# Performance work log

Hardware: AMD Instinct MI355X
Metric: run time of the kernel (lower is better)

## Reference

```python
import jax, jax.numpy as jnp
import numpy as np

B, N, D_IN, D_OUT, MAX_POS = 256, 256, 768, 300, 256
NEG_INF = -9e15
LEAKY_SLOPE = 0.2


def setup_inputs() -> dict:
    key = jax.random.key(0)
    ks = jax.random.split(key, 6)
    h = jax.random.normal(ks[0], (B, N, D_IN), dtype=jnp.float32)
    adj = (jax.random.uniform(ks[1], (B, N, N)) > 0.9).astype(jnp.float32)
    adj = jnp.maximum(adj, jnp.eye(N, dtype=jnp.float32)[None])
    positions = jax.random.randint(ks[2], (B, N), 0, MAX_POS)
    W = jax.random.normal(ks[3], (D_IN, D_OUT), dtype=jnp.float32) * (1.0 / np.sqrt(D_IN))
    a_src = jax.random.normal(ks[4], (1, D_OUT), dtype=jnp.float32) * 0.05
    a_dst = jax.random.normal(ks[5], (1, D_OUT), dtype=jnp.float32) * 0.05
    pos_table = jax.random.normal(jax.random.fold_in(key, 7), (MAX_POS, D_OUT), dtype=jnp.float32)
    return {"h": h, "adj": adj, "positions": positions, "W": W,
            "a_src": a_src, "a_dst": a_dst, "pos_table": pos_table}


def reference(h, adj, positions, W, a_src, a_dst, pos_table):
    # Wh = W(h) + position embedding          [B, N, D_OUT]
    Wh = jnp.einsum('bni,io->bno', h, W) + pos_table[positions]
    # additive attention scores
    f_src = jnp.einsum('bno,o->bn', Wh, a_src[0])  # [B, N]
    f_dst = jnp.einsum('bno,o->bn', Wh, a_dst[0])  # [B, N]
    e = f_src[:, :, None] + f_dst[:, None, :]      # [B, N, N]
    e = jnp.where(e >= 0, e, LEAKY_SLOPE * e)      # LeakyReLU(0.2)
    # adjacency masking + softmax over last dim
    masked = jnp.where(adj > 0, e, NEG_INF)
    attention = jax.nn.softmax(masked, axis=-1)
    # (eval mode: edge dropout and dropout are identity)
    h_prime = jnp.einsum('bnm,bmo->bno', attention, Wh)
    return h_prime, attention
```

## Files before the change

### kernel.cpp

```cpp
#include <hip/hip_runtime.h>

#define B_    256
#define N_    256
#define DIN   768
#define DOUT  300
#define DOUTP 320
#define NT    20
#define M_    (B_*N_)
#define HP_ELEMS (M_*DOUT)
#define NEG_INF -9.0e15f

typedef _Float16 f16;
typedef __attribute__((ext_vector_type(8))) _Float16 f16x8;
typedef __attribute__((ext_vector_type(4))) _Float16 f16x4;
typedef __attribute__((ext_vector_type(4))) float    f32x4;

__device__ __forceinline__ void async_copy16(void* lds, const void* g) {
    __builtin_amdgcn_global_load_lds(
        (const __attribute__((address_space(1))) void*)g,
        (__attribute__((address_space(3))) void*)lds, 16, 0, 0);
}

__global__ __launch_bounds__(256) void prep_wt(const float* __restrict__ W,
                                               f16* __restrict__ Wt) {
    int idx = blockIdx.x * 256 + threadIdx.x;
    if (idx >= DOUTP * DIN) return;
    int n = idx / DIN, k = idx - n * DIN;
    float v = (n < DOUT) ? W[k * DOUT + n] : 0.0f;
    Wt[idx] = (f16)v;
}

__global__ __launch_bounds__(256, 3) void gemm1(
    const float* __restrict__ h, const f16* __restrict__ Wt,
    const int* __restrict__ positions,
    const float* __restrict__ a_src, const float* __restrict__ a_dst,
    const float* __restrict__ pos_table,
    f16* __restrict__ WhT, float* __restrict__ f_src, float* __restrict__ f_dst)
{
    __shared__ f16 Al[64 * 40];
    __shared__ f16 Bl[DOUTP * 32];
    __shared__ float pfs[64][2], pfd[64][2];

    const int tid  = threadIdx.x;
    const int wave = tid >> 6, lane = tid & 63;
    const int quad = lane >> 4, c = lane & 15;
    const int rh = wave & 1;
    const int chf = wave >> 1;
    const int rowbase = blockIdx.x * 64;

    const int brow = lane >> 2;
    const int bj   = (lane & 3) ^ (brow & 3);

    const int ar = tid >> 2, aj = tid & 3;

    f32x4 acc[2][10];
#pragma unroll
    for (int rt = 0; rt < 2; ++rt)
#pragma unroll
        for (int i = 0; i < 10; ++i) acc[rt][i] = (f32x4){0.f, 0.f, 0.f, 0.f};

    for (int kt = 0; kt < DIN / 32; ++kt) {
#pragma unroll
        for (int i = 0; i < 5; ++i) {
            int chk = wave + 4 * i;
            int n = chk * 16 + brow;
            async_copy16((char*)Bl + chk * 1024,
                         Wt + (size_t)n * DIN + kt * 32 + bj * 8);
        }
        {
            const float4* src = (const float4*)(h + (size_t)(rowbase + ar) * DIN + kt * 32 + aj * 8);
            float4 v0 = src[0], v1 = src[1];
            *(f16x8*)&Al[ar * 40 + aj * 8] =
                (f16x8){(f16)v0.x, (f16)v0.y, (f16)v0.z, (f16)v0.w,
                        (f16)v1.x, (f16)v1.y, (f16)v1.z, (f16)v1.w};
        }
        __syncthreads();

        f16x8 af0 = *(const f16x8*)&Al[(rh * 32 + c) * 40 + quad * 8];
        f16x8 af1 = *(const f16x8*)&Al[(rh * 32 + 16 + c) * 40 + quad * 8];
#pragma unroll
        for (int i = 0; i < 10; ++i) {
            int n = (chf * 10 + i) * 16 + c;
            f16x8 bf = *(const f16x8*)&Bl[n * 32 + (quad ^ (n & 3)) * 8];
            acc[0][i] = __builtin_amdgcn_mfma_f32_16x16x32_f16(af0, bf, acc[0][i], 0, 0, 0);
            acc[1][i] = __builtin_amdgcn_mfma_f32_16x16x32_f16(af1, bf, acc[1][i], 0, 0, 0);
        }
        __syncthreads();
    }

    const int bidx  = rowbase >> 8;
    const int mloc  = (rowbase & 255);

    int posr[2][4];
#pragma unroll
    for (int rt = 0; rt < 2; ++rt)
#pragma unroll
        for (int r = 0; r < 4; ++r)
            posr[rt][r] = positions[rowbase + rh * 32 + rt * 16 + quad * 4 + r];

    float fs[2][4] = {{0,0,0,0},{0,0,0,0}}, fd[2][4] = {{0,0,0,0},{0,0,0,0}};
#pragma unroll
    for (int i = 0; i < 10; ++i) {
        int col = (chf * 10 + i) * 16 + c;
        if (col < DOUT) {
            float as = a_src[col], ad = a_dst[col];
#pragma unroll
            for (int rt = 0; rt < 2; ++rt)
#pragma unroll
                for (int r = 0; r < 4; ++r) {
                    float v = acc[rt][i][r] + pos_table[posr[rt][r] * DOUT + col];
                    acc[rt][i][r] = v;
                    fs[rt][r] += v * as;
                    fd[rt][r] += v * ad;
                }
        } else {
#pragma unroll
            for (int rt = 0; rt < 2; ++rt)
#pragma unroll
                for (int r = 0; r < 4; ++r) acc[rt][i][r] = 0.0f;
        }
    }
#pragma unroll
    for (int off = 1; off < 16; off <<= 1) {
#pragma unroll
        for (int rt = 0; rt < 2; ++rt)
#pragma unroll
            for (int r = 0; r < 4; ++r) {
                fs[rt][r] += __shfl_xor(fs[rt][r], off, 16);
                fd[rt][r] += __shfl_xor(fd[rt][r], off, 16);
            }
    }
    if (c == 0) {
#pragma unroll
        for (int rt = 0; rt < 2; ++rt)
#pragma unroll
            for (int r = 0; r < 4; ++r) {
                int row = rh * 32 + rt * 16 + quad * 4 + r;
                pfs[row][chf] = fs[rt][r];
                pfd[row][chf] = fd[rt][r];
            }
    }
#pragma unroll
    for (int i = 0; i < 10; ++i) {
        int col = (chf * 10 + i) * 16 + c;
#pragma unroll
        for (int rt = 0; rt < 2; ++rt) {
            int mrow = mloc + rh * 32 + rt * 16 + quad * 4;
            f16x4 u = (f16x4){(f16)acc[rt][i][0], (f16)acc[rt][i][1],
                              (f16)acc[rt][i][2], (f16)acc[rt][i][3]};
            *(f16x4*)(WhT + ((size_t)bidx * DOUTP + col) * N_ + mrow) = u;
        }
    }
    __syncthreads();
    if (tid < 64) {
        f_src[rowbase + tid] = pfs[tid][0] + pfs[tid][1];
        f_dst[rowbase + tid] = pfd[tid][0] + pfd[tid][1];
    }
}

__global__ __launch_bounds__(256) void softmax_att(
    const float* __restrict__ adj, const float* __restrict__ f_src,
    const float* __restrict__ f_dst, float* __restrict__ att)
{
    const int wave = threadIdx.x >> 6, lane = threadIdx.x & 63;
    const int row = blockIdx.x * 4 + wave;
    const int b = row >> 8;

    float fs = f_src[row];
    float4 fd4 = *(const float4*)(f_dst + b * N_ + lane * 4);
    float4 a4  = *(const float4*)(adj + (size_t)row * N_ + lane * 4);

    float e[4];
    {
        float v;
        v = fs + fd4.x; v = v >= 0.f ? v : 0.2f * v; e[0] = a4.x > 0.f ? v : NEG_INF;
        v = fs + fd4.y; v = v >= 0.f ? v : 0.2f * v; e[1] = a4.y > 0.f ? v : NEG_INF;
        v = fs + fd4.z; v = v >= 0.f ? v : 0.2f * v; e[2] = a4.z > 0.f ? v : NEG_INF;
        v = fs + fd4.w; v = v >= 0.f ? v : 0.2f * v; e[3] = a4.w > 0.f ? v : NEG_INF;
    }
    float mx = fmaxf(fmaxf(e[0], e[1]), fmaxf(e[2], e[3]));
#pragma unroll
    for (int off = 1; off < 64; off <<= 1) mx = fmaxf(mx, __shfl_xor(mx, off, 64));

    float p[4], s = 0.f;
#pragma unroll
    for (int i = 0; i < 4; ++i) { p[i] = __expf(e[i] - mx); s += p[i]; }
#pragma unroll
    for (int off = 1; off < 64; off <<= 1) s += __shfl_xor(s, off, 64);

    float inv = 1.0f / s;
    *(float4*)(att + (size_t)row * N_ + lane * 4) =
        make_float4(p[0] * inv, p[1] * inv, p[2] * inv, p[3] * inv);
}

__global__ __launch_bounds__(256, 3) void gemm2(
    const float* __restrict__ att, const f16* __restrict__ WhT,
    float* __restrict__ hp)
{
    __shared__ f16 Al[64 * 40];
    __shared__ f16 Bl[DOUTP * 32];

    const int tid  = threadIdx.x;
    const int wave = tid >> 6, lane = tid & 63;
    const int quad = lane >> 4, c = lane & 15;
    const int rh = wave & 1;
    const int chf = wave >> 1;
    const int rowbase = blockIdx.x * 64;
    const int bidx = rowbase >> 8;

    const int brow = lane >> 2;
    const int bj   = (lane & 3) ^ (brow & 3);
    const int ar = tid >> 2, aj = tid & 3;

    f32x4 acc[2][10];
#pragma unroll
    for (int rt = 0; rt < 2; ++rt)
#pragma unroll
        for (int i = 0; i < 10; ++i) acc[rt][i] = (f32x4){0.f, 0.f, 0.f, 0.f};

    for (int kt = 0; kt < N_ / 32; ++kt) {
#pragma unroll
        for (int i = 0; i < 5; ++i) {
            int chk = wave + 4 * i;
            int n = chk * 16 + brow;
            async_copy16((char*)Bl + chk * 1024,
                         WhT + ((size_t)bidx * DOUTP + n) * N_ + kt * 32 + bj * 8);
        }
        {
            const float4* src = (const float4*)(att + (size_t)(rowbase + ar) * N_ + kt * 32 + aj * 8);
            float4 v0 = src[0], v1 = src[1];
            *(f16x8*)&Al[ar * 40 + aj * 8] =
                (f16x8){(f16)v0.x, (f16)v0.y, (f16)v0.z, (f16)v0.w,
                        (f16)v1.x, (f16)v1.y, (f16)v1.z, (f16)v1.w};
        }
        __syncthreads();

        f16x8 af0 = *(const f16x8*)&Al[(rh * 32 + c) * 40 + quad * 8];
        f16x8 af1 = *(const f16x8*)&Al[(rh * 32 + 16 + c) * 40 + quad * 8];
#pragma unroll
        for (int i = 0; i < 10; ++i) {
            int n = (chf * 10 + i) * 16 + c;
            f16x8 bf = *(const f16x8*)&Bl[n * 32 + (quad ^ (n & 3)) * 8];
            acc[0][i] = __builtin_amdgcn_mfma_f32_16x16x32_f16(af0, bf, acc[0][i], 0, 0, 0);
            acc[1][i] = __builtin_amdgcn_mfma_f32_16x16x32_f16(af1, bf, acc[1][i], 0, 0, 0);
        }
        __syncthreads();
    }

#pragma unroll
    for (int i = 0; i < 10; ++i) {
        int col = (chf * 10 + i) * 16 + c;
        if (col < DOUT) {
#pragma unroll
            for (int rt = 0; rt < 2; ++rt) {
                int row0 = rowbase + rh * 32 + rt * 16 + quad * 4;
#pragma unroll
                for (int r = 0; r < 4; ++r)
                    hp[(size_t)(row0 + r) * DOUT + col] = acc[rt][i][r];
            }
        }
    }
}

extern "C" void kernel_launch(void* const* d_in, const int* in_sizes, int n_in,
                              void* d_out, int out_size, void* d_ws, size_t ws_size,
                              hipStream_t stream)
{
    const float* h         = (const float*)d_in[0];
    const float* adj       = (const float*)d_in[1];
    const int*   positions = (const int*)d_in[2];
    const float* W         = (const float*)d_in[3];
    const float* a_src     = (const float*)d_in[4];
    const float* a_dst     = (const float*)d_in[5];
    const float* pos_table = (const float*)d_in[6];

    float* hp  = (float*)d_out;
    float* att = hp + HP_ELEMS;

    f16*   Wt    = (f16*)d_ws;
    f16*   WhT   = Wt + (size_t)DOUTP * DIN;
    float* f_src = (float*)(WhT + (size_t)B_ * DOUTP * N_);
    float* f_dst = f_src + M_;

    hipLaunchKernelGGL(prep_wt,     dim3((DOUTP * DIN + 255) / 256), dim3(256), 0, stream, W, Wt);
    hipLaunchKernelGGL(gemm1,       dim3(M_ / 64),  dim3(256), 0, stream,
                       h, Wt, positions, a_src, a_dst, pos_table, WhT, f_src, f_dst);
    hipLaunchKernelGGL(softmax_att, dim3(M_ / 4),   dim3(256), 0, stream, adj, f_src, f_dst, att);
    hipLaunchKernelGGL(gemm2,       dim3(M_ / 64),  dim3(256), 0, stream, att, WhT, hp);
}
```

Baseline: 469.9 us.

## Fuse softmax into second GEMM and software-pipeline first GEMM's loads

The softmax kernel is merged into the attention-times-Wh GEMM. Each block computes its 64 rows of attention probabilities, writes them to global memory and keeps an fp16 copy in LDS for the GEMM, so the attention matrix is not re-read from memory. The first GEMM is restructured with triple-buffered B tiles, double-buffered A tiles and manual waitcnt/barrier placement so global loads overlap MFMA work. Occupancy is lowered to 2 blocks per CU to make room for the larger LDS footprint.

```diff
diff --git a/kernel.cpp b/kernel.cpp
--- a/kernel.cpp
+++ b/kernel.cpp
@@ -5,7 +5,6 @@
 #define DIN   768
 #define DOUT  300
 #define DOUTP 320
-#define NT    20
 #define M_    (B_*N_)
 #define HP_ELEMS (M_*DOUT)
 #define NEG_INF -9.0e15f
@@ -30,15 +29,15 @@
     Wt[idx] = (f16)v;
 }
 
-__global__ __launch_bounds__(256, 3) void gemm1(
+__global__ __launch_bounds__(256, 2) void gemm1(
     const float* __restrict__ h, const f16* __restrict__ Wt,
     const int* __restrict__ positions,
     const float* __restrict__ a_src, const float* __restrict__ a_dst,
     const float* __restrict__ pos_table,
     f16* __restrict__ WhT, float* __restrict__ f_src, float* __restrict__ f_dst)
 {
-    __shared__ f16 Al[64 * 40];
-    __shared__ f16 Bl[DOUTP * 32];
+    __shared__ f16 Al[2][64 * 40];
+    __shared__ f16 Bl[3][DOUTP * 32];
     __shared__ float pfs[64][2], pfd[64][2];
 
     const int tid  = threadIdx.x;
@@ -50,43 +49,94 @@
 
     const int brow = lane >> 2;
     const int bj   = (lane & 3) ^ (brow & 3);
-
     const int ar = tid >> 2, aj = tid & 3;
 
+    const float* abase = h + (size_t)(rowbase + ar) * DIN + aj * 8;
+
     f32x4 acc[2][10];
 #pragma unroll
     for (int rt = 0; rt < 2; ++rt)
 #pragma unroll
         for (int i = 0; i < 10; ++i) acc[rt][i] = (f32x4){0.f, 0.f, 0.f, 0.f};
 
-    for (int kt = 0; kt < DIN / 32; ++kt) {
-#pragma unroll
-        for (int i = 0; i < 5; ++i) {
-            int chk = wave + 4 * i;
-            int n = chk * 16 + brow;
-            async_copy16((char*)Bl + chk * 1024,
-                         Wt + (size_t)n * DIN + kt * 32 + bj * 8);
-        }
-        {
-            const float4* src = (const float4*)(h + (size_t)(rowbase + ar) * DIN + kt * 32 + aj * 8);
-            float4 v0 = src[0], v1 = src[1];
-            *(f16x8*)&Al[ar * 40 + aj * 8] =
-                (f16x8){(f16)v0.x, (f16)v0.y, (f16)v0.z, (f16)v0.w,
-                        (f16)v1.x, (f16)v1.y, (f16)v1.z, (f16)v1.w};
-        }
-        __syncthreads();
-
-        f16x8 af0 = *(const f16x8*)&Al[(rh * 32 + c) * 40 + quad * 8];
-        f16x8 af1 = *(const f16x8*)&Al[(rh * 32 + 16 + c) * 40 + quad * 8];
-#pragma unroll
-        for (int i = 0; i < 10; ++i) {
-            int n = (chf * 10 + i) * 16 + c;
-            f16x8 bf = *(const f16x8*)&Bl[n * 32 + (quad ^ (n & 3)) * 8];
-            acc[0][i] = __builtin_amdgcn_mfma_f32_16x16x32_f16(af0, bf, acc[0][i], 0, 0, 0);
-            acc[1][i] = __builtin_amdgcn_mfma_f32_16x16x32_f16(af1, bf, acc[1][i], 0, 0, 0);
-        }
-        __syncthreads();
-    }
+#define STAGE_B(K, BUF) do {                                                   \
+    _Pragma("unroll")                                                          \
+    for (int i_ = 0; i_ < 5; ++i_) {                                           \
+        int chk_ = wave + 4 * i_;                                              \
+        int n_ = chk_ * 16 + brow;                                             \
+        async_copy16((char*)Bl[(BUF)] + chk_ * 1024,                           \
+                     Wt + (size_t)n_ * DIN + (size_t)(K) * 32 + bj * 8);       \
+    } } while (0)
+
+#define LOAD_A(K, V0, V1) do {                                                 \
+    const float4* s_ = (const float4*)(abase + (size_t)(K) * 32);              \
+    V0 = s_[0]; V1 = s_[1]; } while (0)
+
+#define WRITE_A(BUF, V0, V1)                                                   \
+    *(f16x8*)&Al[(BUF)][ar * 40 + aj * 8] =                                    \
+        (f16x8){(f16)V0.x, (f16)V0.y, (f16)V0.z, (f16)V0.w,                    \
+                (f16)V1.x, (f16)V1.y, (f16)V1.z, (f16)V1.w}
+
+    float4 r0a, r0b, r1a, r1b;
+
+    STAGE_B(0, 0); LOAD_A(0, r0a, r0b);
+    asm volatile("" ::: "memory");
+    STAGE_B(1, 1); LOAD_A(1, r1a, r1b);
+    WRITE_A(0, r0a, r0b);
+    asm volatile("s_waitcnt vmcnt(7)" ::: "memory");
+    asm volatile("s_waitcnt lgkmcnt(0)" ::: "memory");
+    __builtin_amdgcn_s_barrier();
+    asm volatile("" ::: "memory");
+
+#define ITER(KT, CB, NB, CA, PF, WA, BAR) do {                                 \
+    if (PF) {                                                                  \
+        STAGE_B((KT) + 2, NB);                                                 \
+        if ((CA) == 0) { LOAD_A((KT) + 2, r0a, r0b); }                         \
+        else           { LOAD_A((KT) + 2, r1a, r1b); }                         \
+    }                                                                          \
+    {                                                                          \
+        f16x8 af0 = *(const f16x8*)&Al[(CA)][(rh * 32 + c) * 40 + quad * 8];   \
+        f16x8 af1 = *(const f16x8*)&Al[(CA)][(rh * 32 + 16 + c) * 40 + quad * 8]; \
+        _Pragma("unroll")                                                      \
+        for (int i_ = 0; i_ < 10; ++i_) {                                      \
+            int n_ = (chf * 10 + i_) * 16 + c;                                 \
+            f16x8 bf = *(const f16x8*)&Bl[(CB)][n_ * 32 + (quad ^ (n_ & 3)) * 8]; \
+            acc[0][i_] = __builtin_amdgcn_mfma_f32_16x16x32_f16(af0, bf, acc[0][i_], 0, 0, 0); \
+            acc[1][i_] = __builtin_amdgcn_mfma_f32_16x16x32_f16(af1, bf, acc[1][i_], 0, 0, 0); \
+        }                                                                      \
+    }                                                                          \
+    if (WA) {                                                                  \
+        if ((CA) == 0) { WRITE_A((CA) ^ 1, r1a, r1b); }                        \
+        else           { WRITE_A((CA) ^ 1, r0a, r0b); }                        \
+    }                                                                          \
+    if (BAR) {                                                                 \
+        if (PF) { asm volatile("s_waitcnt vmcnt(7)" ::: "memory"); }           \
+        else    { asm volatile("s_waitcnt vmcnt(0)" ::: "memory"); }           \
+        asm volatile("s_waitcnt lgkmcnt(0)" ::: "memory");                     \
+        __builtin_amdgcn_s_barrier();                                          \
+        asm volatile("" ::: "memory");                                         \
+    }                                                                          \
+} while (0)
+
+    for (int kb = 0; kb < 18; kb += 6) {
+        ITER(kb + 0, 0, 2, 0, 1, 1, 1);
+        ITER(kb + 1, 1, 0, 1, 1, 1, 1);
+        ITER(kb + 2, 2, 1, 0, 1, 1, 1);
+        ITER(kb + 3, 0, 2, 1, 1, 1, 1);
+        ITER(kb + 4, 1, 0, 0, 1, 1, 1);
+        ITER(kb + 5, 2, 1, 1, 1, 1, 1);
+    }
+    ITER(18, 0, 2, 0, 1, 1, 1);
+    ITER(19, 1, 0, 1, 1, 1, 1);
+    ITER(20, 2, 1, 0, 1, 1, 1);
+    ITER(21, 0, 2, 1, 1, 1, 1);
+    ITER(22, 1, 0, 0, 0, 1, 1);
+    ITER(23, 2, 1, 1, 0, 0, 0);
+
+#undef ITER
+#undef WRITE_A
+#undef LOAD_A
+#undef STAGE_B
 
     const int bidx  = rowbase >> 8;
     const int mloc  = (rowbase & 255);
@@ -158,47 +208,13 @@
     }
 }
 
-__global__ __launch_bounds__(256) void softmax_att(
+__global__ __launch_bounds__(256, 2) void fused2(
     const float* __restrict__ adj, const float* __restrict__ f_src,
-    const float* __restrict__ f_dst, float* __restrict__ att)
+    const float* __restrict__ f_dst, const f16* __restrict__ WhT,
+    float* __restrict__ att, float* __restrict__ hp)
 {
-    const int wave = threadIdx.x >> 6, lane = threadIdx.x & 63;
-    const int row = blockIdx.x * 4 + wave;
-    const int b = row >> 8;
-
-    float fs = f_src[row];
-    float4 fd4 = *(const float4*)(f_dst + b * N_ + lane * 4);
-    float4 a4  = *(const float4*)(adj + (size_t)row * N_ + lane * 4);
-
-    float e[4];
-    {
-        float v;
-        v = fs + fd4.x; v = v >= 0.f ? v : 0.2f * v; e[0] = a4.x > 0.f ? v : NEG_INF;
-        v = fs + fd4.y; v = v >= 0.f ? v : 0.2f * v; e[1] = a4.y > 0.f ? v : NEG_INF;
-        v = fs + fd4.z; v = v >= 0.f ? v : 0.2f * v; e[2] = a4.z > 0.f ? v : NEG_INF;
-        v = fs + fd4.w; v = v >= 0.f ? v : 0.2f * v; e[3] = a4.w > 0.f ? v : NEG_INF;
-    }
-    float mx = fmaxf(fmaxf(e[0], e[1]), fmaxf(e[2], e[3]));
-#pragma unroll
-    for (int off = 1; off < 64; off <<= 1) mx = fmaxf(mx, __shfl_xor(mx, off, 64));
-
-    float p[4], s = 0.f;
-#pragma unroll
-    for (int i = 0; i < 4; ++i) { p[i] = __expf(e[i] - mx); s += p[i]; }
-#pragma unroll
-    for (int off = 1; off < 64; off <<= 1) s += __shfl_xor(s, off, 64);
-
-    float inv = 1.0f / s;
-    *(float4*)(att + (size_t)row * N_ + lane * 4) =
-        make_float4(p[0] * inv, p[1] * inv, p[2] * inv, p[3] * inv);
-}
-
-__global__ __launch_bounds__(256, 3) void gemm2(
-    const float* __restrict__ att, const f16* __restrict__ WhT,
-    float* __restrict__ hp)
-{
-    __shared__ f16 Al[64 * 40];
-    __shared__ f16 Bl[DOUTP * 32];
+    __shared__ f16 Pl[64 * 264];
+    __shared__ f16 Bl[2][DOUTP * 32];
 
     const int tid  = threadIdx.x;
     const int wave = tid >> 6, lane = tid & 63;
@@ -210,7 +226,54 @@
 
     const int brow = lane >> 2;
     const int bj   = (lane & 3) ^ (brow & 3);
-    const int ar = tid >> 2, aj = tid & 3;
+
+#define STAGE_B2(K, BUF) do {                                                  \
+    _Pragma("unroll")                                                          \
+    for (int i_ = 0; i_ < 5; ++i_) {                                           \
+        int chk_ = wave + 4 * i_;                                              \
+        int n_ = chk_ * 16 + brow;                                             \
+        async_copy16((char*)Bl[(BUF)] + chk_ * 1024,                           \
+                     WhT + ((size_t)bidx * DOUTP + n_) * N_ + (size_t)(K) * 32 + bj * 8); \
+    } } while (0)
+
+    STAGE_B2(0, 0);
+    STAGE_B2(1, 1);
+
+    {
+        float4 fd4 = *(const float4*)(f_dst + bidx * N_ + lane * 4);
+        const float* arow = adj + (size_t)(rowbase + wave * 16) * N_ + lane * 4;
+        float4 nx = *(const float4*)arow;
+        for (int rr = 0; rr < 16; ++rr) {
+            float4 a4 = nx;
+            if (rr < 15) nx = *(const float4*)(arow + (size_t)(rr + 1) * N_);
+            const int lrow = wave * 16 + rr;
+            const int row  = rowbase + lrow;
+            float fs = f_src[row];
+
+            float v, e0, e1, e2, e3;
+            v = fs + fd4.x; v = v >= 0.f ? v : 0.2f * v; e0 = a4.x > 0.f ? v : NEG_INF;
+            v = fs + fd4.y; v = v >= 0.f ? v : 0.2f * v; e1 = a4.y > 0.f ? v : NEG_INF;
+            v = fs + fd4.z; v = v >= 0.f ? v : 0.2f * v; e2 = a4.z > 0.f ? v : NEG_INF;
+            v = fs + fd4.w; v = v >= 0.f ? v : 0.2f * v; e3 = a4.w > 0.f ? v : NEG_INF;
+
+            float mx = fmaxf(fmaxf(e0, e1), fmaxf(e2, e3));
+#pragma unroll
+            for (int off = 1; off < 64; off <<= 1) mx = fmaxf(mx, __shfl_xor(mx, off, 64));
+
+            float p0 = __expf(e0 - mx), p1 = __expf(e1 - mx);
+            float p2 = __expf(e2 - mx), p3 = __expf(e3 - mx);
+            float s = p0 + p1 + p2 + p3;
+#pragma unroll
+            for (int off = 1; off < 64; off <<= 1) s += __shfl_xor(s, off, 64);
+
+            float inv = 1.0f / s;
+            *(float4*)(att + (size_t)row * N_ + lane * 4) =
+                make_float4(p0 * inv, p1 * inv, p2 * inv, p3 * inv);
+            *(f16x4*)&Pl[lrow * 264 + lane * 4] =
+                (f16x4){(f16)(p0 * inv), (f16)(p1 * inv), (f16)(p2 * inv), (f16)(p3 * inv)};
+        }
+    }
+    __syncthreads();
 
     f32x4 acc[2][10];
 #pragma unroll
@@ -218,34 +281,23 @@
 #pragma unroll
         for (int i = 0; i < 10; ++i) acc[rt][i] = (f32x4){0.f, 0.f, 0.f, 0.f};
 
-    for (int kt = 0; kt < N_ / 32; ++kt) {
-#pragma unroll
-        for (int i = 0; i < 5; ++i) {
-            int chk = wave + 4 * i;
-            int n = chk * 16 + brow;
-            async_copy16((char*)Bl + chk * 1024,
-                         WhT + ((size_t)bidx * DOUTP + n) * N_ + kt * 32 + bj * 8);
-        }
-        {
-            const float4* src = (const float4*)(att + (size_t)(rowbase + ar) * N_ + kt * 32 + aj * 8);
-            float4 v0 = src[0], v1 = src[1];
-            *(f16x8*)&Al[ar * 40 + aj * 8] =
-                (f16x8){(f16)v0.x, (f16)v0.y, (f16)v0.z, (f16)v0.w,
-                        (f16)v1.x, (f16)v1.y, (f16)v1.z, (f16)v1.w};
-        }
-        __syncthreads();
-
-        f16x8 af0 = *(const f16x8*)&Al[(rh * 32 + c) * 40 + quad * 8];
-        f16x8 af1 = *(const f16x8*)&Al[(rh * 32 + 16 + c) * 40 + quad * 8];
+#pragma unroll
+    for (int kt = 0; kt < 8; ++kt) {
+        f16x8 af0 = *(const f16x8*)&Pl[(rh * 32 + c) * 264 + kt * 32 + quad * 8];
+        f16x8 af1 = *(const f16x8*)&Pl[(rh * 32 + 16 + c) * 264 + kt * 32 + quad * 8];
 #pragma unroll
         for (int i = 0; i < 10; ++i) {
             int n = (chf * 10 + i) * 16 + c;
-            f16x8 bf = *(const f16x8*)&Bl[n * 32 + (quad ^ (n & 3)) * 8];
+            f16x8 bf = *(const f16x8*)&Bl[kt & 1][n * 32 + (quad ^ (n & 3)) * 8];
             acc[0][i] = __builtin_amdgcn_mfma_f32_16x16x32_f16(af0, bf, acc[0][i], 0, 0, 0);
             acc[1][i] = __builtin_amdgcn_mfma_f32_16x16x32_f16(af1, bf, acc[1][i], 0, 0, 0);
         }
-        __syncthreads();
-    }
+        if (kt < 7) {
+            __syncthreads();
+            if (kt + 2 < 8) STAGE_B2(kt + 2, kt & 1);
+        }
+    }
+#undef STAGE_B2
 
 #pragma unroll
     for (int i = 0; i < 10; ++i) {
@@ -282,9 +334,9 @@
     float* f_src = (float*)(WhT + (size_t)B_ * DOUTP * N_);
     float* f_dst = f_src + M_;
 
-    hipLaunchKernelGGL(prep_wt,     dim3((DOUTP * DIN + 255) / 256), dim3(256), 0, stream, W, Wt);
-    hipLaunchKernelGGL(gemm1,       dim3(M_ / 64),  dim3(256), 0, stream,
+    hipLaunchKernelGGL(prep_wt, dim3((DOUTP * DIN + 255) / 256), dim3(256), 0, stream, W, Wt);
+    hipLaunchKernelGGL(gemm1,   dim3(M_ / 64), dim3(256), 0, stream,
                        h, Wt, positions, a_src, a_dst, pos_table, WhT, f_src, f_dst);
-    hipLaunchKernelGGL(softmax_att, dim3(M_ / 4),   dim3(256), 0, stream, adj, f_src, f_dst, att);
-    hipLaunchKernelGGL(gemm2,       dim3(M_ / 64),  dim3(256), 0, stream, att, WhT, hp);
-}
+    hipLaunchKernelGGL(fused2,  dim3(M_ / 64), dim3(256), 0, stream,
+                       adj, f_src, f_dst, WhT, att, hp);
+}
```

Measured after the change: 448.7 us. -4.5%, faster.
